# Optimization experiments

Hardware: AMD Instinct MI355X
Metric: run time of the kernel (lower is better)

The kernel has to match this reference:

```python
import jax, jax.numpy as jnp
import numpy as np

EPS = 1e-5
NUM_HEADS = 8
KEY_DIM = 16
D = 64  # attn_ratio * key_dim


def conv1x1_bn(x, w, g, b, m, v):
    # x: (B, Cin, H, W), w: (Cout, Cin); eval-mode BatchNorm over channel dim
    y = jnp.einsum('bchw,oc->bohw', x, w)
    scale = (g * jax.lax.rsqrt(v + EPS))[None, :, None, None]
    shift = (b - g * m * jax.lax.rsqrt(v + EPS))[None, :, None, None]
    return y * scale + shift


def setup_inputs() -> dict:
    key = jax.random.key(0)
    ks = jax.random.split(key, 22)
    dim, nh_kd, dh = 384, 128, 512
    f = jax.random.normal
    u = jax.random.uniform
    return {
        'x': f(ks[0], (2, dim, 56, 56), jnp.float32),
        'wq': f(ks[1], (nh_kd, dim), jnp.float32) * 0.05,
        'qg': u(ks[2], (nh_kd,), jnp.float32), 'qb': f(ks[3], (nh_kd,)) * 0.1,
        'qm': f(ks[4], (nh_kd,)) * 0.1, 'qv': u(ks[5], (nh_kd,)) + 0.5,
        'wk': f(ks[6], (nh_kd, dim), jnp.float32) * 0.05,
        'kg': u(ks[7], (nh_kd,), jnp.float32), 'kb': f(ks[8], (nh_kd,)) * 0.1,
        'km': f(ks[9], (nh_kd,)) * 0.1, 'kvv': u(ks[10], (nh_kd,)) + 0.5,
        'wv': f(ks[11], (dh, dim), jnp.float32) * 0.05,
        'vg': u(ks[12], (dh,), jnp.float32), 'vb': f(ks[13], (dh,)) * 0.1,
        'vm': f(ks[14], (dh,)) * 0.1, 'vvv': u(ks[15], (dh,)) + 0.5,
        'wp': f(ks[16], (dim, dh), jnp.float32) * 0.05,
        'pg': u(ks[17], (dim,), jnp.float32), 'pb': f(ks[18], (dim,)) * 0.1,
        'pm': f(ks[19], (dim,)) * 0.1, 'pvv': u(ks[20], (dim,)) + 0.5,
    }


def reference(x, wq, qg, qb, qm, qv, wk, kg, kb, km, kvv,
              wv, vg, vb, vm, vvv, wp, pg, pb, pm, pvv):
    B, C, H, W = x.shape
    N = H * W
    h, kd, d = NUM_HEADS, KEY_DIM, D
    # (B, h, N, kd)
    qq = conv1x1_bn(x, wq, qg, qb, qm, qv).reshape(B, h, kd, N).transpose(0, 1, 3, 2)
    # (B, h, kd, N)
    kk = conv1x1_bn(x, wk, kg, kb, km, kvv).reshape(B, h, kd, N)
    # (B, h, N, d)
    vv = conv1x1_bn(x, wv, vg, vb, vm, vvv).reshape(B, h, d, N).transpose(0, 1, 3, 2)
    # NOTE: original forward does NOT apply self.scale
    attn = jax.nn.softmax(jnp.matmul(qq, kk), axis=-1)  # (B, h, N, N)
    xx = jnp.matmul(attn, vv)                            # (B, h, N, d)
    xx = xx.transpose(0, 1, 3, 2).reshape(B, h * d, H, W)
    xx = jax.nn.relu(xx)
    return conv1x1_bn(xx, wp, pg, pb, pm, pvv)
```

## Files before the change

### kernel.cpp

```cpp
#include <hip/hip_runtime.h>
#include <hip/hip_bf16.h>

#define B_   2
#define CIN  384
#define NPIX 3136
#define NH   8
#define KD   16
#define DHEAD 64
#define NHKD 128
#define QKW  256
#define DHD  512
#define EPSW 1e-5f

typedef __attribute__((ext_vector_type(8))) short vshort8;
typedef __attribute__((ext_vector_type(4))) short vshort4;
typedef __attribute__((ext_vector_type(4))) float vfloat4;
typedef __attribute__((ext_vector_type(16))) float vfloat16;

static __device__ __forceinline__ float bf2f(short s) {
    unsigned int u = ((unsigned int)(unsigned short)s) << 16;
    return __builtin_bit_cast(float, u);
}
static __device__ __forceinline__ short f2bf(float f) {
    unsigned int u = __builtin_bit_cast(unsigned int, f);
    unsigned int lsb = (u >> 16) & 1u;
    u += 0x7fffu + lsb;
    return (short)(u >> 16);
}
static __device__ __forceinline__ float pget(const void* p, int i, int f32) {
    return f32 ? ((const float*)p)[i] : bf2f(((const short*)p)[i]);
}

static __device__ __forceinline__ int detect_f32(const unsigned short* x) {
    int lane = threadIdx.x & 63;
    bool big = false;
#pragma unroll
    for (int j = 0; j < 8; j++) {
        int e = (x[(lane * 8 + j) * 2] >> 7) & 0xFF;
        big = big || (e >= 0xC0);
    }
    unsigned long long bal = __ballot(big);
    return __popcll(bal) >= 32;
}

__global__ __launch_bounds__(256) void prep_kernel(
    const void* __restrict__ x,
    const void* __restrict__ wq, const void* __restrict__ wk,
    const void* __restrict__ wv, const void* __restrict__ wp,
    short* __restrict__ wB, short* __restrict__ xT,
    const void* qg, const void* qb, const void* qm, const void* qv,
    const void* kg, const void* kb, const void* km, const void* kv,
    const void* vg, const void* vb, const void* vm, const void* vv,
    const void* pg, const void* pb, const void* pm, const void* pv,
    float* __restrict__ scA, float* __restrict__ shA)
{
    __shared__ short tile[32][33];
    int f32 = detect_f32((const unsigned short*)x);
    int id = blockIdx.x;
    int t = threadIdx.x;

    if (id < 1920) {
        int i = id * 256 + t;
        const void* src; int j;
        if (i < 49152)       { src = wq; j = i; }
        else if (i < 98304)  { src = wk; j = i - 49152; }
        else if (i < 294912) { src = wv; j = i - 98304; }
        else                 { src = wp; j = i - 294912; }
        wB[i] = f32 ? f2bf(((const float*)src)[j]) : ((const short*)src)[j];
        if (i < 1152) {
            const void *g, *bb, *mn, *vr;
            if (i < 128)      { g = qg; bb = qb; mn = qm; vr = qv; j = i; }
            else if (i < 256) { g = kg; bb = kb; mn = km; vr = kv; j = i - 128; }
            else if (i < 768) { g = vg; bb = vb; mn = vm; vr = vv; j = i - 256; }
            else              { g = pg; bb = pb; mn = pm; vr = pv; j = i - 768; }
            float iv = rsqrtf(pget(vr, j, f32) + EPSW);
            float s = pget(g, j, f32) * iv;
            scA[i] = s;
            shA[i] = pget(bb, j, f32) - pget(mn, j, f32) * s;
        }
        return;
    }

    int tid2 = id - 1920;
    int b = tid2 / 1176, rr = tid2 % 1176;
    int n0 = (rr % 98) * 32, c0 = (rr / 98) * 32;
    int r = t >> 3, q4 = (t & 7) * 4;
    size_t off = ((size_t)b * CIN + c0 + r) * NPIX + n0 + q4;
    if (f32) {
        float4 v = *(const float4*)((const float*)x + off);
        tile[r][q4 + 0] = f2bf(v.x);
        tile[r][q4 + 1] = f2bf(v.y);
        tile[r][q4 + 2] = f2bf(v.z);
        tile[r][q4 + 3] = f2bf(v.w);
    } else {
        vshort4 v = *(const vshort4*)((const short*)x + off);
#pragma unroll
        for (int i = 0; i < 4; i++) tile[r][q4 + i] = v[i];
    }
    __syncthreads();
    vshort4 o;
#pragma unroll
    for (int i = 0; i < 4; i++) o[i] = tile[q4 + i][r];
    *(vshort4*)(xT + ((size_t)b * NPIX + n0 + r) * CIN + c0 + q4) = o;
}

static __device__ __forceinline__ void gemm_body(
    short* Al, short* Bl,
    const short* __restrict__ A, const short* __restrict__ Bt,
    void* __restrict__ C, size_t coff, int m0, int n0,
    const float* __restrict__ sc, const float* __restrict__ sh,
    int Nb, int K, int bnPerRow, int finalOut, int f32)
{
    int t = threadIdx.x, lane = t & 63, w = t >> 6, m = lane & 15, quad = lane >> 4;
    int srow = t >> 2, scol = (t & 3) * 16;
    const short* ag = A + (size_t)(m0 + srow) * K + scol;
    const short* bg = Bt + (size_t)(n0 + srow) * K + scol;
    vfloat4 acc[4];
#pragma unroll
    for (int i = 0; i < 4; i++) acc[i] = (vfloat4){0.f, 0.f, 0.f, 0.f};

    for (int k0 = 0; k0 < K; k0 += 64) {
        vshort8 a0 = *(const vshort8*)(ag + k0);
        vshort8 a1 = *(const vshort8*)(ag + k0 + 8);
        vshort8 b0 = *(const vshort8*)(bg + k0);
        vshort8 b1 = *(const vshort8*)(bg + k0 + 8);
        __syncthreads();
        *(vshort8*)&Al[srow * 72 + scol] = a0;
        *(vshort8*)&Al[srow * 72 + scol + 8] = a1;
        *(vshort8*)&Bl[srow * 72 + scol] = b0;
        *(vshort8*)&Bl[srow * 72 + scol + 8] = b1;
        __syncthreads();
#pragma unroll
        for (int kk = 0; kk < 2; kk++) {
            vshort8 af = *(const vshort8*)&Al[(w * 16 + m) * 72 + kk * 32 + quad * 8];
#pragma unroll
            for (int nc = 0; nc < 4; nc++) {
                vshort8 bf = *(const vshort8*)&Bl[(nc * 16 + m) * 72 + kk * 32 + quad * 8];
                acc[nc] = __builtin_amdgcn_mfma_f32_16x16x32_bf16(af, bf, acc[nc], 0, 0, 0);
            }
        }
    }

#pragma unroll
    for (int nc = 0; nc < 4; nc++) {
        int col = n0 + nc * 16 + m;
        float scc = bnPerRow ? 0.f : sc[col];
        float shc = bnPerRow ? 0.f : sh[col];
#pragma unroll
        for (int r = 0; r < 4; r++) {
            int row = m0 + w * 16 + quad * 4 + r;
            float s2 = bnPerRow ? sc[row] : scc;
            float h2 = bnPerRow ? sh[row] : shc;
            float val = s2 * acc[nc][r] + h2;
            size_t idx = coff + (size_t)row * Nb + col;
            if (finalOut && f32) ((float*)C)[idx] = val;
            else                 ((short*)C)[idx] = f2bf(val);
        }
    }
}

__global__ __launch_bounds__(256) void proj_kernel(
    const short* __restrict__ xT, const short* __restrict__ wqkB,
    const short* __restrict__ wvB, short* __restrict__ QKt,
    short* __restrict__ Vb,
    const float* __restrict__ scA, const float* __restrict__ shA)
{
    __shared__ __attribute__((aligned(16))) short Al[64 * 72];
    __shared__ __attribute__((aligned(16))) short Bl[64 * 72];
    int id = blockIdx.x;
    if (id < 392) {
        int b = id / 196, r = id % 196;
        int m0 = (r % 49) * 64, n0 = (r / 49) * 64;
        gemm_body(Al, Bl, xT + (size_t)b * NPIX * CIN, wqkB,
                  QKt, (size_t)b * NPIX * QKW, m0, n0,
                  scA, shA, QKW, CIN, 0, 0, 0);
    } else {
        id -= 392;
        int b = id / 392, r = id % 392;
        int m0 = (r % 8) * 64, n0 = (r / 8) * 64;
        gemm_body(Al, Bl, wvB, xT + (size_t)b * NPIX * CIN,
                  Vb, (size_t)b * DHD * NPIX, m0, n0,
                  scA + 256, shA + 256, NPIX, CIN, 1, 0, 0);
    }
}

__global__ __launch_bounds__(256) void pgemm_kernel(
    const short* __restrict__ wpB, const short* __restrict__ xx,
    void* __restrict__ out,
    const float* __restrict__ scA, const float* __restrict__ shA,
    const void* __restrict__ x)
{
    __shared__ __attribute__((aligned(16))) short Al[64 * 72];
    __shared__ __attribute__((aligned(16))) short Bl[64 * 72];
    int f32 = detect_f32((const unsigned short*)x);
    int id = blockIdx.x;
    int b = id / 294, r = id % 294;
    int m0 = (r % 6) * 64, n0 = (r / 6) * 64;
    gemm_body(Al, Bl, wpB, xx + (size_t)b * NPIX * DHD,
              out, (size_t)b * CIN * NPIX, m0, n0,
              scA + 768, shA + 768, NPIX, DHD, 1, 1, f32);
}

__global__ __launch_bounds__(128) void attn_kernel(
    const short* __restrict__ QKt, const short* __restrict__ V,
    short* __restrict__ xx)
{
    __shared__ __attribute__((aligned(16))) short Kl[2][64 * 16];
    __shared__ __attribute__((aligned(16))) short Vl[2][64 * 72];
    __shared__ __attribute__((aligned(16))) short Pl[64 * 72];
    int bh = blockIdx.y, b = bh >> 3, h = bh & 7;
    int q0 = blockIdx.x * 64;
    int t = threadIdx.x, lane = t & 63, w = t >> 6;
    int c31 = lane & 31, half = lane >> 5;

    int q = q0 + w * 32 + c31;
    vshort8 aq = *(const vshort8*)(QKt + ((size_t)b * NPIX + q) * QKW + h * KD + half * 8);

    vfloat16 o0, o1, oL, z16;
#pragma unroll
    for (int i = 0; i < 16; i++) { o0[i] = 0.f; o1[i] = 0.f; oL[i] = 0.f; z16[i] = 0.f; }

    int kkey = t >> 1, kofs = (t & 1) * 8;
    const short* kgp = QKt + (size_t)b * NPIX * QKW + NHKD + h * KD + kofs;
    int vd = t >> 1, vkh = (t & 1) * 32;
    const short* vgp = V + ((size_t)(b * DHD) + h * DHEAD + vd) * NPIX + vkh;
    const short one_bf = (short)0x3F80;
    const vshort8 ones = {one_bf, one_bf, one_bf, one_bf, one_bf, one_bf, one_bf, one_bf};

    *(vshort8*)&Kl[0][kkey * 16 + kofs] = *(const vshort8*)(kgp + (size_t)kkey * QKW);
#pragma unroll
    for (int i = 0; i < 4; i++)
        *(vshort8*)&Vl[0][vd * 72 + vkh + i * 8] = *(const vshort8*)(vgp + i * 8);
    __syncthreads();

    for (int it = 0; it < NPIX / 64; ++it) {
        int cur = it & 1, nxt = cur ^ 1;
        int k0 = it * 64;
        bool more = (it + 1) < (NPIX / 64);
        vshort8 ks, vs[4];
        if (more) {
            ks = *(const vshort8*)(kgp + (size_t)(k0 + 64 + kkey) * QKW);
#pragma unroll
            for (int i = 0; i < 4; i++)
                vs[i] = *(const vshort8*)(vgp + k0 + 64 + i * 8);
        }

        short* pw = &Pl[(w * 32 + c31) * 72];
#pragma unroll
        for (int kg = 0; kg < 2; kg++) {
            vshort8 ak = *(const vshort8*)&Kl[cur][(kg * 32 + c31) * 16 + half * 8];
            vfloat16 s = __builtin_amdgcn_mfma_f32_32x32x16_bf16(ak, aq, z16, 0, 0, 0);
#pragma unroll
            for (int rb = 0; rb < 4; rb++) {
                vshort4 pv;
#pragma unroll
                for (int j = 0; j < 4; j++) {
                    float p = __expf(s[rb * 4 + j]);
                    pv[j] = (short)(__builtin_bit_cast(unsigned int, p) >> 16);
                }
                *(vshort4*)&pw[kg * 32 + half * 4 + rb * 8] = pv;
            }
        }

#pragma unroll
        for (int kc = 0; kc < 4; kc++) {
            vshort8 ap  = *(const vshort8*)&Pl[(w * 32 + c31) * 72 + kc * 16 + half * 8];
            vshort8 bv0 = *(const vshort8*)&Vl[cur][(c31) * 72 + kc * 16 + half * 8];
            vshort8 bv1 = *(const vshort8*)&Vl[cur][(32 + c31) * 72 + kc * 16 + half * 8];
            o0 = __builtin_amdgcn_mfma_f32_32x32x16_bf16(ap, bv0, o0, 0, 0, 0);
            o1 = __builtin_amdgcn_mfma_f32_32x32x16_bf16(ap, bv1, o1, 0, 0, 0);
            oL = __builtin_amdgcn_mfma_f32_32x32x16_bf16(ap, ones, oL, 0, 0, 0);
        }

        if (more) {
            *(vshort8*)&Kl[nxt][kkey * 16 + kofs] = ks;
#pragma unroll
            for (int i = 0; i < 4; i++)
                *(vshort8*)&Vl[nxt][vd * 72 + vkh + i * 8] = vs[i];
        }
        __syncthreads();
    }

#pragma unroll
    for (int r = 0; r < 16; r++) {
        int ql = (r & 3) + 8 * (r >> 2) + 4 * half;
        int qrow = q0 + w * 32 + ql;
        float inv = 1.0f / oL[r];
        size_t base = ((size_t)b * NPIX + qrow) * DHD + h * DHEAD + c31;
        xx[base]      = f2bf(fmaxf(o0[r] * inv, 0.f));
        xx[base + 32] = f2bf(fmaxf(o1[r] * inv, 0.f));
    }
}

extern "C" void kernel_launch(void* const* d_in, const int* in_sizes, int n_in,
                              void* d_out, int out_size, void* d_ws, size_t ws_size,
                              hipStream_t stream) {
    const void* x  = d_in[0];
    const void* wq = d_in[1];
    const void* qg = d_in[2];  const void* qb = d_in[3];
    const void* qm = d_in[4];  const void* qv = d_in[5];
    const void* wk = d_in[6];
    const void* kg = d_in[7];  const void* kb = d_in[8];
    const void* km = d_in[9];  const void* kv = d_in[10];
    const void* wv = d_in[11];
    const void* vg = d_in[12]; const void* vb = d_in[13];
    const void* vm = d_in[14]; const void* vv = d_in[15];
    const void* wp = d_in[16];
    const void* pg = d_in[17]; const void* pb = d_in[18];
    const void* pm = d_in[19]; const void* pv = d_in[20];

    short* xT  = (short*)d_ws;
    short* wB  = xT + (size_t)B_ * NPIX * CIN;
    short* wqkB = wB;
    short* wvB  = wB + 98304;
    short* wpB  = wB + 294912;
    short* QKt = wB + 491520;
    short* Vb  = QKt + (size_t)B_ * NPIX * QKW;
    short* xx  = Vb + (size_t)B_ * DHD * NPIX;
    float* scA = (float*)(xx + (size_t)B_ * NPIX * DHD);
    float* shA = scA + 1152;

    prep_kernel<<<4272, 256, 0, stream>>>(
        x, wq, wk, wv, wp, wB, xT,
        qg, qb, qm, qv, kg, kb, km, kv,
        vg, vb, vm, vv, pg, pb, pm, pv, scA, shA);

    proj_kernel<<<1176, 256, 0, stream>>>(xT, wqkB, wvB, QKt, Vb, scA, shA);

    attn_kernel<<<dim3(NPIX / 64, B_ * NH), 128, 0, stream>>>(QKt, Vb, xx);

    pgemm_kernel<<<588, 256, 0, stream>>>(wpB, xx, d_out, scA, shA, x);
}
```

Baseline: 198.9 us.

## Split attention keys across wave pairs, keep P in registers via permlane swap

The attention kernel now runs 256 threads per block, with two wave pairs each processing alternate 64-key chunks (split-K). K and V fragments are loaded straight from global memory into registers instead of being staged through LDS. The softmax probabilities are packed with v_cvt_pk_bf16_f32 and rearranged with permlane32_swap into the MFMA A-operand layout, removing the P round trip through shared memory. Partial outputs and row sums are combined across the pairs through LDS at the end. This drops the per-iteration barriers and doubles parallelism, but it relies on uncoalesced direct global loads and adds a reduction step.

```diff
diff --git a/kernel.cpp b/kernel.cpp
--- a/kernel.cpp
+++ b/kernel.cpp
@@ -16,6 +16,8 @@
 typedef __attribute__((ext_vector_type(4))) short vshort4;
 typedef __attribute__((ext_vector_type(4))) float vfloat4;
 typedef __attribute__((ext_vector_type(16))) float vfloat16;
+typedef __attribute__((ext_vector_type(4))) unsigned int vuint4;
+typedef __attribute__((ext_vector_type(2))) int vint2;
 
 static __device__ __forceinline__ float bf2f(short s) {
     unsigned int u = ((unsigned int)(unsigned short)s) << 16;
@@ -29,6 +31,11 @@
 }
 static __device__ __forceinline__ float pget(const void* p, int i, int f32) {
     return f32 ? ((const float*)p)[i] : bf2f(((const short*)p)[i]);
+}
+static __device__ __forceinline__ unsigned int cvtpk(float lo, float hi) {
+    unsigned int r;
+    asm("v_cvt_pk_bf16_f32 %0, %1, %2" : "=v"(r) : "v"(lo), "v"(hi));
+    return r;
 }
 
 static __device__ __forceinline__ int detect_f32(const unsigned short* x) {
@@ -201,94 +208,103 @@
               scA + 768, shA + 768, NPIX, DHD, 1, 1, f32);
 }
 
-__global__ __launch_bounds__(128) void attn_kernel(
+__global__ __launch_bounds__(256) void attn_kernel(
     const short* __restrict__ QKt, const short* __restrict__ V,
     short* __restrict__ xx)
 {
-    __shared__ __attribute__((aligned(16))) short Kl[2][64 * 16];
-    __shared__ __attribute__((aligned(16))) short Vl[2][64 * 72];
-    __shared__ __attribute__((aligned(16))) short Pl[64 * 72];
+    __shared__ float ex[2][2][32][64];
+
     int bh = blockIdx.y, b = bh >> 3, h = bh & 7;
     int q0 = blockIdx.x * 64;
     int t = threadIdx.x, lane = t & 63, w = t >> 6;
     int c31 = lane & 31, half = lane >> 5;
-
-    int q = q0 + w * 32 + c31;
+    int p = w & 1;
+    int par = w >> 1;
+    int nt = 25 - par;
+
+    int q = q0 + p * 32 + c31;
     vshort8 aq = *(const vshort8*)(QKt + ((size_t)b * NPIX + q) * QKW + h * KD + half * 8);
 
+    const short* kp = QKt + ((size_t)b * NPIX + c31) * QKW + NHKD + h * KD + half * 8;
+    const short* vp0 = V + ((size_t)(b * DHD) + h * DHEAD + c31) * NPIX + half * 8;
+    const short* vp1 = vp0 + (size_t)32 * NPIX;
+
     vfloat16 o0, o1, oL, z16;
 #pragma unroll
     for (int i = 0; i < 16; i++) { o0[i] = 0.f; o1[i] = 0.f; oL[i] = 0.f; z16[i] = 0.f; }
-
-    int kkey = t >> 1, kofs = (t & 1) * 8;
-    const short* kgp = QKt + (size_t)b * NPIX * QKW + NHKD + h * KD + kofs;
-    int vd = t >> 1, vkh = (t & 1) * 32;
-    const short* vgp = V + ((size_t)(b * DHD) + h * DHEAD + vd) * NPIX + vkh;
     const short one_bf = (short)0x3F80;
     const vshort8 ones = {one_bf, one_bf, one_bf, one_bf, one_bf, one_bf, one_bf, one_bf};
 
-    *(vshort8*)&Kl[0][kkey * 16 + kofs] = *(const vshort8*)(kgp + (size_t)kkey * QKW);
-#pragma unroll
-    for (int i = 0; i < 4; i++)
-        *(vshort8*)&Vl[0][vd * 72 + vkh + i * 8] = *(const vshort8*)(vgp + i * 8);
+    int k0 = par * 64;
+    vshort8 kf0 = *(const vshort8*)(kp + (size_t)k0 * QKW);
+    vshort8 kf1 = *(const vshort8*)(kp + (size_t)(k0 + 32) * QKW);
+
+    for (int i = 0; i < nt; i++) {
+        vshort8 vf[8];
+#pragma unroll
+        for (int kc = 0; kc < 4; kc++) {
+            vf[kc * 2]     = *(const vshort8*)(vp0 + k0 + kc * 16);
+            vf[kc * 2 + 1] = *(const vshort8*)(vp1 + k0 + kc * 16);
+        }
+        vshort8 kn0 = kf0, kn1 = kf1;
+        if (i + 1 < nt) {
+            kn0 = *(const vshort8*)(kp + (size_t)(k0 + 128) * QKW);
+            kn1 = *(const vshort8*)(kp + (size_t)(k0 + 160) * QKW);
+        }
+
+#pragma unroll
+        for (int kg = 0; kg < 2; kg++) {
+            vfloat16 s = __builtin_amdgcn_mfma_f32_32x32x16_bf16(kg ? kf1 : kf0, aq, z16, 0, 0, 0);
+            unsigned int pk[8];
+#pragma unroll
+            for (int j = 0; j < 8; j++) {
+                float plo = __expf(s[2 * j]);
+                float phi = __expf(s[2 * j + 1]);
+                pk[j] = cvtpk(plo, phi);
+            }
+#pragma unroll
+            for (int kc2 = 0; kc2 < 2; kc2++) {
+                int kc = kg * 2 + kc2, o = kc2 * 4;
+                vint2 s0 = __builtin_amdgcn_permlane32_swap((int)pk[o + 0], (int)pk[o + 2], false, false);
+                vint2 s1 = __builtin_amdgcn_permlane32_swap((int)pk[o + 1], (int)pk[o + 3], false, false);
+                vuint4 fr;
+                fr[0] = (unsigned int)s0[0]; fr[1] = (unsigned int)s1[0];
+                fr[2] = (unsigned int)s0[1]; fr[3] = (unsigned int)s1[1];
+                vshort8 ap = __builtin_bit_cast(vshort8, fr);
+                o0 = __builtin_amdgcn_mfma_f32_32x32x16_bf16(ap, vf[kc * 2],     o0, 0, 0, 0);
+                o1 = __builtin_amdgcn_mfma_f32_32x32x16_bf16(ap, vf[kc * 2 + 1], o1, 0, 0, 0);
+                oL = __builtin_amdgcn_mfma_f32_32x32x16_bf16(ap, ones,           oL, 0, 0, 0);
+            }
+        }
+        kf0 = kn0; kf1 = kn1;
+        k0 += 128;
+    }
+
+    if (par == 1) {
+#pragma unroll
+        for (int r = 0; r < 16; r++) {
+            ex[1][p][r][lane]      = o0[r];
+            ex[1][p][16 + r][lane] = oL[r];
+        }
+    } else {
+#pragma unroll
+        for (int r = 0; r < 16; r++) {
+            ex[0][p][r][lane]      = o1[r];
+            ex[0][p][16 + r][lane] = oL[r];
+        }
+    }
     __syncthreads();
 
-    for (int it = 0; it < NPIX / 64; ++it) {
-        int cur = it & 1, nxt = cur ^ 1;
-        int k0 = it * 64;
-        bool more = (it + 1) < (NPIX / 64);
-        vshort8 ks, vs[4];
-        if (more) {
-            ks = *(const vshort8*)(kgp + (size_t)(k0 + 64 + kkey) * QKW);
-#pragma unroll
-            for (int i = 0; i < 4; i++)
-                vs[i] = *(const vshort8*)(vgp + k0 + 64 + i * 8);
-        }
-
-        short* pw = &Pl[(w * 32 + c31) * 72];
-#pragma unroll
-        for (int kg = 0; kg < 2; kg++) {
-            vshort8 ak = *(const vshort8*)&Kl[cur][(kg * 32 + c31) * 16 + half * 8];
-            vfloat16 s = __builtin_amdgcn_mfma_f32_32x32x16_bf16(ak, aq, z16, 0, 0, 0);
-#pragma unroll
-            for (int rb = 0; rb < 4; rb++) {
-                vshort4 pv;
-#pragma unroll
-                for (int j = 0; j < 4; j++) {
-                    float p = __expf(s[rb * 4 + j]);
-                    pv[j] = (short)(__builtin_bit_cast(unsigned int, p) >> 16);
-                }
-                *(vshort4*)&pw[kg * 32 + half * 4 + rb * 8] = pv;
-            }
-        }
-
-#pragma unroll
-        for (int kc = 0; kc < 4; kc++) {
-            vshort8 ap  = *(const vshort8*)&Pl[(w * 32 + c31) * 72 + kc * 16 + half * 8];
-            vshort8 bv0 = *(const vshort8*)&Vl[cur][(c31) * 72 + kc * 16 + half * 8];
-            vshort8 bv1 = *(const vshort8*)&Vl[cur][(32 + c31) * 72 + kc * 16 + half * 8];
-            o0 = __builtin_amdgcn_mfma_f32_32x32x16_bf16(ap, bv0, o0, 0, 0, 0);
-            o1 = __builtin_amdgcn_mfma_f32_32x32x16_bf16(ap, bv1, o1, 0, 0, 0);
-            oL = __builtin_amdgcn_mfma_f32_32x32x16_bf16(ap, ones, oL, 0, 0, 0);
-        }
-
-        if (more) {
-            *(vshort8*)&Kl[nxt][kkey * 16 + kofs] = ks;
-#pragma unroll
-            for (int i = 0; i < 4; i++)
-                *(vshort8*)&Vl[nxt][vd * 72 + vkh + i * 8] = vs[i];
-        }
-        __syncthreads();
-    }
-
 #pragma unroll
     for (int r = 0; r < 16; r++) {
+        float ov, Lv;
+        if (par == 0) { ov = o0[r] + ex[1][p][r][lane]; Lv = oL[r] + ex[1][p][16 + r][lane]; }
+        else          { ov = o1[r] + ex[0][p][r][lane]; Lv = oL[r] + ex[0][p][16 + r][lane]; }
         int ql = (r & 3) + 8 * (r >> 2) + 4 * half;
-        int qrow = q0 + w * 32 + ql;
-        float inv = 1.0f / oL[r];
-        size_t base = ((size_t)b * NPIX + qrow) * DHD + h * DHEAD + c31;
-        xx[base]      = f2bf(fmaxf(o0[r] * inv, 0.f));
-        xx[base + 32] = f2bf(fmaxf(o1[r] * inv, 0.f));
+        int qrow = q0 + p * 32 + ql;
+        float inv = 1.0f / Lv;
+        size_t base = ((size_t)b * NPIX + qrow) * DHD + h * DHEAD + (par ? 32 : 0) + c31;
+        xx[base] = f2bf(fmaxf(ov * inv, 0.f));
     }
 }
 
@@ -327,7 +343,7 @@
 
     proj_kernel<<<1176, 256, 0, stream>>>(xT, wqkB, wvB, QKt, Vb, scA, shA);
 
-    attn_kernel<<<dim3(NPIX / 64, B_ * NH), 128, 0, stream>>>(QKt, Vb, xx);
+    attn_kernel<<<dim3(NPIX / 64, B_ * NH), 256, 0, stream>>>(QKt, Vb, xx);
 
     pgemm_kernel<<<588, 256, 0, stream>>>(wpB, xx, d_out, scA, shA, x);
 }
```

After: 252.4 us. +26.9%, slower.

## Split attention over key range into two partial passes plus combine kernel

Applied to the files above, without the earlier changes.

Splits the attention key loop into two halves via a third grid dimension, so each block accumulates unnormalized output and row sums over half the keys and writes fp32 partials. A new combine kernel sums the partials, normalizes, applies ReLU and writes bf16 activations. This doubles the attention grid (784 to 1568 blocks of 128 threads) to raise occupancy and CU utilization on the long sequential key loop. In exchange it adds fp32 partial-output traffic (about 25 MB written and read back) and an extra kernel launch. The split needs no max-rescaling because the kernel uses unshifted exponentials.

```diff
diff --git a/kernel.cpp b/kernel.cpp
--- a/kernel.cpp
+++ b/kernel.cpp
@@ -203,13 +203,14 @@
 
 __global__ __launch_bounds__(128) void attn_kernel(
     const short* __restrict__ QKt, const short* __restrict__ V,
-    short* __restrict__ xx)
+    float* __restrict__ Op, float* __restrict__ Lp)
 {
     __shared__ __attribute__((aligned(16))) short Kl[2][64 * 16];
     __shared__ __attribute__((aligned(16))) short Vl[2][64 * 72];
     __shared__ __attribute__((aligned(16))) short Pl[64 * 72];
     int bh = blockIdx.y, b = bh >> 3, h = bh & 7;
     int q0 = blockIdx.x * 64;
+    int z = blockIdx.z;
     int t = threadIdx.x, lane = t & 63, w = t >> 6;
     int c31 = lane & 31, half = lane >> 5;
 
@@ -227,16 +228,19 @@
     const short one_bf = (short)0x3F80;
     const vshort8 ones = {one_bf, one_bf, one_bf, one_bf, one_bf, one_bf, one_bf, one_bf};
 
-    *(vshort8*)&Kl[0][kkey * 16 + kofs] = *(const vshort8*)(kgp + (size_t)kkey * QKW);
+    int kbase = z * 25 * 64;
+    int nt = z ? 24 : 25;
+
+    *(vshort8*)&Kl[0][kkey * 16 + kofs] = *(const vshort8*)(kgp + (size_t)(kbase + kkey) * QKW);
 #pragma unroll
     for (int i = 0; i < 4; i++)
-        *(vshort8*)&Vl[0][vd * 72 + vkh + i * 8] = *(const vshort8*)(vgp + i * 8);
+        *(vshort8*)&Vl[0][vd * 72 + vkh + i * 8] = *(const vshort8*)(vgp + kbase + i * 8);
     __syncthreads();
 
-    for (int it = 0; it < NPIX / 64; ++it) {
+    for (int it = 0; it < nt; ++it) {
         int cur = it & 1, nxt = cur ^ 1;
-        int k0 = it * 64;
-        bool more = (it + 1) < (NPIX / 64);
+        int k0 = kbase + it * 64;
+        bool more = (it + 1) < nt;
         vshort8 ks, vs[4];
         if (more) {
             ks = *(const vshort8*)(kgp + (size_t)(k0 + 64 + kkey) * QKW);
@@ -285,11 +289,35 @@
     for (int r = 0; r < 16; r++) {
         int ql = (r & 3) + 8 * (r >> 2) + 4 * half;
         int qrow = q0 + w * 32 + ql;
-        float inv = 1.0f / oL[r];
-        size_t base = ((size_t)b * NPIX + qrow) * DHD + h * DHEAD + c31;
-        xx[base]      = f2bf(fmaxf(o0[r] * inv, 0.f));
-        xx[base + 32] = f2bf(fmaxf(o1[r] * inv, 0.f));
-    }
+        size_t pb = (((size_t)z * 16 + bh) * NPIX + qrow) * 64 + c31;
+        Op[pb]      = o0[r];
+        Op[pb + 32] = o1[r];
+        if (c31 == 0) Lp[((size_t)z * 16 + bh) * NPIX + qrow] = oL[r];
+    }
+}
+
+__global__ __launch_bounds__(256) void attn_combine(
+    const float* __restrict__ Op, const float* __restrict__ Lp,
+    short* __restrict__ xx)
+{
+    int idx = blockIdx.x * 256 + threadIdx.x;
+    int d4 = idx & 15;
+    int rest = idx >> 4;
+    int qq = rest % NPIX, bh = rest / NPIX;
+    const size_t zO = (size_t)16 * NPIX * 64;
+    const size_t zL = (size_t)16 * NPIX;
+    size_t base = ((size_t)bh * NPIX + qq) * 64 + d4 * 4;
+    float4 a = *(const float4*)(Op + base);
+    float4 c = *(const float4*)(Op + base + zO);
+    float L = Lp[(size_t)bh * NPIX + qq] + Lp[zL + (size_t)bh * NPIX + qq];
+    float inv = 1.0f / L;
+    int b = bh >> 3, h = bh & 7;
+    vshort4 o;
+    o[0] = f2bf(fmaxf((a.x + c.x) * inv, 0.f));
+    o[1] = f2bf(fmaxf((a.y + c.y) * inv, 0.f));
+    o[2] = f2bf(fmaxf((a.z + c.z) * inv, 0.f));
+    o[3] = f2bf(fmaxf((a.w + c.w) * inv, 0.f));
+    *(vshort4*)&xx[((size_t)b * NPIX + qq) * DHD + h * DHEAD + d4 * 4] = o;
 }
 
 extern "C" void kernel_launch(void* const* d_in, const int* in_sizes, int n_in,
@@ -319,6 +347,8 @@
     short* xx  = Vb + (size_t)B_ * DHD * NPIX;
     float* scA = (float*)(xx + (size_t)B_ * NPIX * DHD);
     float* shA = scA + 1152;
+    float* Op  = shA + 1152;
+    float* Lp  = Op + (size_t)2 * 16 * NPIX * 64;
 
     prep_kernel<<<4272, 256, 0, stream>>>(
         x, wq, wk, wv, wp, wB, xT,
@@ -327,7 +357,9 @@
 
     proj_kernel<<<1176, 256, 0, stream>>>(xT, wqkB, wvB, QKt, Vb, scA, shA);
 
-    attn_kernel<<<dim3(NPIX / 64, B_ * NH), 128, 0, stream>>>(QKt, Vb, xx);
+    attn_kernel<<<dim3(NPIX / 64, B_ * NH, 2), 128, 0, stream>>>(QKt, Vb, Op, Lp);
+
+    attn_combine<<<3136, 256, 0, stream>>>(Op, Lp, xx);
 
     pgemm_kernel<<<588, 256, 0, stream>>>(wpB, xx, d_out, scA, shA, x);
 }
```

After: 204.0 us. 2.6% more time.
